# Performance work log

Hardware: AMD Instinct MI355X
Metric: run time of the kernel (lower is better)

Reference implementation:

```python
import jax, jax.numpy as jnp
import numpy as np

EPS = 1e-5
NEG_SLOPE = 0.2


def knn(x, k):
    # x: (B, C, N). pairwise_distance = -||xi - xj||^2, topk -> nearest neighbors.
    xt = jnp.swapaxes(x, 1, 2)                       # (B, N, C)
    inner = -2.0 * jnp.matmul(xt, x)                 # (B, N, N)
    xx = jnp.sum(x * x, axis=1, keepdims=True)       # (B, 1, N)
    pd = -xx - inner - jnp.swapaxes(xx, 1, 2)        # (B, N, N)
    return jax.lax.top_k(pd, k)[1]                   # (B, N, k) int32


def get_graph_feature(x, k):
    # x: (B, C, N) -> (B, N, k, 2C) edge features [neighbor - center, center]
    idx = knn(x, k)
    xt = jnp.swapaxes(x, 1, 2)                       # (B, N, C)
    nb = jax.vmap(lambda f, i: f[i])(xt, idx)        # (B, N, k, C) gather
    center = xt[:, :, None, :]                       # (B, N, 1, C)
    return jnp.concatenate(
        [nb - center, jnp.broadcast_to(center, nb.shape)], axis=-1)


def edge_conv(x, w, k):
    # conv_2d with kernel 1: 1x1 conv (no bias) + InstanceNorm2d + LeakyReLU, then max over k
    feat = get_graph_feature(x, k)                   # (B, N, k, 2C)
    y = jnp.einsum('bnkc,oc->bonk', feat, w)         # (B, O, N, k)
    mean = jnp.mean(y, axis=(2, 3), keepdims=True)
    var = jnp.var(y, axis=(2, 3), keepdims=True)
    y = (y - mean) * jax.lax.rsqrt(var + EPS)        # InstanceNorm2d (no affine)
    y = jnp.where(y >= 0, y, NEG_SLOPE * y)
    return jnp.max(y, axis=-1)                       # (B, O, N)


def setup_inputs() -> dict:
    key = jax.random.key(0)
    ks = jax.random.split(key, 8)
    B, N = 16, 2048
    s = 0.05
    return {
        'x': jax.random.normal(ks[0], (B, 3, N), dtype=jnp.float32),
        'w1': jax.random.normal(ks[1], (64, 6), dtype=jnp.float32) * s,
        'w2': jax.random.normal(ks[2], (64, 128), dtype=jnp.float32) * s,
        'w3': jax.random.normal(ks[3], (128, 128), dtype=jnp.float32) * s,
        'w4': jax.random.normal(ks[4], (256, 256), dtype=jnp.float32) * s,
        'w5': jax.random.normal(ks[5], (512, 512), dtype=jnp.float32) * s,
        'bn5_gamma': jnp.ones((512,), dtype=jnp.float32),
        'bn5_beta': jnp.zeros((512,), dtype=jnp.float32),
    }


def reference(x, w1, w2, w3, w4, w5, bn5_gamma, bn5_beta):
    k = 20
    x1 = edge_conv(x, w1, k)                         # (B, 64, N)
    x2 = edge_conv(x1, w2, k)                        # (B, 64, N)
    x3 = edge_conv(x2, w3, k)                        # (B, 128, N)
    x4 = edge_conv(x3, w4, k)                        # (B, 256, N)
    x_cat = jnp.concatenate([x1, x2, x3, x4], axis=1)  # (B, 512, N)
    y = jnp.einsum('bcn,oc->bon', x_cat, w5)         # conv5, (B, 512, N)
    # BatchNorm1d (training-mode batch stats) over (B, N)
    mean = jnp.mean(y, axis=(0, 2), keepdims=True)
    var = jnp.var(y, axis=(0, 2), keepdims=True)
    y = (y - mean) * jax.lax.rsqrt(var + EPS)
    y = y * bn5_gamma[None, :, None] + bn5_beta[None, :, None]
    y = jnp.where(y >= 0, y, NEG_SLOPE * y)
    feat = jnp.concatenate([jnp.max(y, axis=2), jnp.mean(y, axis=2)], axis=1)  # (B, 1024)
    return feat
```

## Files before the change

kernel.cpp:

```cpp
#include <hip/hip_runtime.h>

#define NN 2048
#define NB 16
#define KK 20
#define EPSF 1e-5f

typedef unsigned long long ull;
typedef _Float16 v8h __attribute__((ext_vector_type(8)));
typedef float v4f __attribute__((ext_vector_type(4)));

__device__ __forceinline__ float shflx_f(float v, int m) { return __shfl_xor(v, m, 64); }
__device__ __forceinline__ ull shflx_u64(ull v, int m) {
  int lo = __shfl_xor((int)(unsigned)v, m, 64);
  int hi = __shfl_xor((int)(unsigned)(v >> 32), m, 64);
  return (((ull)(unsigned)hi) << 32) | (unsigned)lo;
}
__device__ __forceinline__ ull packkey(float s, int n) {
  unsigned u = __float_as_uint(s);
  u = (u & 0x80000000u) ? ~u : (u | 0x80000000u);
  return (((ull)u) << 32) | (unsigned)(2047 - n);
}

__global__ __launch_bounds__(256) void prep_kernel(const float* __restrict__ x,
    _Float16* __restrict__ xh, _Float16* __restrict__ xl, float* __restrict__ xx,
    int C, int KB, long bstride)
{
  const int b = blockIdx.y;
  const int n = blockIdx.x * 256 + threadIdx.x;
  const float* xb = x + (size_t)b * bstride;
  const int Cp = KB * 32;
  _Float16* ph = xh + ((size_t)b * NN + n) * Cp;
  _Float16* pl = xl + ((size_t)b * NN + n) * Cp;
  float s = 0.f;
  for (int kb = 0; kb < KB; kb++) {
    for (int g = 0; g < 4; g++) {
      v8h hv, lv;
#pragma unroll
      for (int j = 0; j < 8; j++) {
        int c = kb * 32 + g * 8 + j;
        float v = (c < C) ? xb[(size_t)c * NN + n] : 0.f;
        _Float16 h = (_Float16)v;
        hv[j] = h;
        lv[j] = (_Float16)(v - (float)h);
        s = fmaf(v, v, s);
      }
      *(v8h*)(ph + kb * 32 + g * 8) = hv;
      *(v8h*)(pl + kb * 32 + g * 8) = lv;
    }
  }
  xx[b * NN + n] = s;
}

template<int KB>
__device__ __forceinline__ void tile_scores(const v8h (&Bh)[KB], const v8h (&Bl)[KB],
    const v8h (&Ah)[4][KB], const v8h (&Al)[4][KB], float xv, v4f (&out)[4])
{
#pragma unroll
  for (int a = 0; a < 4; a++) {
    v4f a0 = {0.f, 0.f, 0.f, 0.f};
    v4f a1 = {0.f, 0.f, 0.f, 0.f};
#pragma unroll
    for (int kb = 0; kb < KB; kb++) {
      v4f& acc = (kb & 1) ? a1 : a0;
      acc = __builtin_amdgcn_mfma_f32_16x16x32_f16(Ah[a][kb], Bh[kb], acc, 0, 0, 0);
      acc = __builtin_amdgcn_mfma_f32_16x16x32_f16(Ah[a][kb], Bl[kb], acc, 0, 0, 0);
      acc = __builtin_amdgcn_mfma_f32_16x16x32_f16(Al[a][kb], Bh[kb], acc, 0, 0, 0);
    }
    v4f s = a0 + a1;
#pragma unroll
    for (int j = 0; j < 4; j++) out[a][j] = s[j] - 0.5f * xv;
  }
}

template<int KB>
__global__ __launch_bounds__(256, 1) void knn2(
    const _Float16* __restrict__ xh, const _Float16* __restrict__ xl,
    const float* __restrict__ xxg, ull* __restrict__ slistG, int* __restrict__ cntG)
{
  __shared__ float gmL[256][33];
  __shared__ float tauL[256];
  __shared__ int scnt[256];

  const int t = threadIdx.x;
  const int lane = t & 63;
  const int wave = t >> 6;
  const int col = lane & 15;
  const int quad = lane >> 4;
  const int quad8 = quad * 8;
  const int b = blockIdx.x >> 1;
  const int chunk = blockIdx.x & 1;
  const int qg = blockIdx.y;
  const int Cp = KB * 32;
  const int cb = chunk * 1024;
  const _Float16* xhb = xh + (size_t)b * NN * Cp;
  const _Float16* xlb = xl + (size_t)b * NN * Cp;
  const float* xxb = xxg + b * NN;

  v8h Ah[4][KB], Al[4][KB];
  const int qw = qg * 256 + wave * 64;
#pragma unroll
  for (int a = 0; a < 4; a++) {
    const _Float16* pa = xhb + (size_t)(qw + a * 16 + col) * Cp + quad8;
    const _Float16* pb = xlb + (size_t)(qw + a * 16 + col) * Cp + quad8;
#pragma unroll
    for (int kb = 0; kb < KB; kb++) {
      Ah[a][kb] = *(const v8h*)(pa + kb * 32);
      Al[a][kb] = *(const v8h*)(pb + kb * 32);
    }
  }

  v8h Bh[2][KB], Bl[2][KB];
  float xvb[2];
  auto loadB = [&](int slot, int tt) {
    int t2 = tt < 63 ? tt : 63;
    int n = cb + t2 * 16 + col;
    const _Float16* pb = xhb + (size_t)n * Cp + quad8;
    const _Float16* pl = xlb + (size_t)n * Cp + quad8;
#pragma unroll
    for (int kb = 0; kb < KB; kb++) {
      Bh[slot][kb] = *(const v8h*)(pb + kb * 32);
      Bl[slot][kb] = *(const v8h*)(pl + kb * 32);
    }
    xvb[slot] = xxb[n];
  };

  float gm[4][8];
#pragma unroll
  for (int a = 0; a < 4; a++)
#pragma unroll
    for (int j = 0; j < 8; j++) gm[a][j] = -3.4e38f;

  loadB(0, 0);
  for (int tt = 0; tt < 64; tt += 2) {
    loadB(1, tt + 1);
    {
      v4f out[4];
      tile_scores<KB>(Bh[0], Bl[0], Ah, Al, xvb[0], out);
#pragma unroll
      for (int a = 0; a < 4; a++)
#pragma unroll
        for (int j = 0; j < 4; j++) gm[a][j * 2] = fmaxf(gm[a][j * 2], out[a][j]);
    }
    loadB(0, tt + 2);
    {
      v4f out[4];
      tile_scores<KB>(Bh[1], Bl[1], Ah, Al, xvb[1], out);
#pragma unroll
      for (int a = 0; a < 4; a++)
#pragma unroll
        for (int j = 0; j < 4; j++) gm[a][j * 2 + 1] = fmaxf(gm[a][j * 2 + 1], out[a][j]);
    }
  }

#pragma unroll
  for (int a = 0; a < 4; a++)
#pragma unroll
    for (int j = 0; j < 4; j++) {
      int qi = wave * 64 + a * 16 + quad * 4 + j;
      gmL[qi][col * 2 + 0] = gm[a][j * 2 + 0];
      gmL[qi][col * 2 + 1] = gm[a][j * 2 + 1];
    }
  scnt[t] = 0;
  asm volatile("s_waitcnt lgkmcnt(0)" ::: "memory");

  for (int r = 0; r < 32; r++) {
    const int q = wave * 64 + r * 2 + (lane >> 5);
    const int idx = lane & 31;
    float v = gmL[q][idx];
#pragma unroll
    for (int kk = 2; kk <= 32; kk <<= 1) {
#pragma unroll
      for (int m = kk >> 1; m >= 1; m >>= 1) {
        float o = shflx_f(v, m);
        bool keepmax = ((idx & kk) == 0) == ((idx & m) == 0);
        v = keepmax ? fmaxf(v, o) : fminf(v, o);
      }
    }
    if (idx == 19) tauL[q] = v;
  }
  asm volatile("s_waitcnt lgkmcnt(0)" ::: "memory");

  float tq[4][4];
#pragma unroll
  for (int a = 0; a < 4; a++)
#pragma unroll
    for (int j = 0; j < 4; j++) tq[a][j] = tauL[wave * 64 + a * 16 + quad * 4 + j];

  ull* slB = slistG + (((size_t)b * NN + qg * 256) * 2 + chunk) * 64;
  loadB(0, 0);
  for (int tt = 0; tt < 64; tt += 2) {
    loadB(1, tt + 1);
    for (int s = 0; s < 2; s++) {
      v4f out[4];
      tile_scores<KB>(s ? Bh[1] : Bh[0], s ? Bl[1] : Bl[0], Ah, Al, xvb[s], out);
      int n = cb + (tt + s) * 16 + col;
#pragma unroll
      for (int a = 0; a < 4; a++)
#pragma unroll
        for (int j = 0; j < 4; j++) {
          float sc = out[a][j];
          if (sc >= tq[a][j]) {
            int qi = wave * 64 + a * 16 + quad * 4 + j;
            int pos = atomicAdd(&scnt[qi], 1);
            if (pos < 64) slB[(size_t)qi * 128 + pos] = packkey(sc, n);
          }
        }
      if (s == 0) loadB(0, tt + 2);
    }
  }
  asm volatile("s_waitcnt lgkmcnt(0)" ::: "memory");
  cntG[((size_t)b * NN + qg * 256 + t) * 2 + chunk] = scnt[t];
}

__global__ __launch_bounds__(256) void knn_merge(const ull* __restrict__ slistG,
    const int* __restrict__ cntG, const _Float16* __restrict__ xh,
    const _Float16* __restrict__ xl, const float* __restrict__ xxg,
    int* __restrict__ idxout, int Cp, int C)
{
  const int lane = threadIdx.x & 63, wave = threadIdx.x >> 6;
  const int b = blockIdx.y;
  const int q = blockIdx.x * 4 + wave;
  const int c0 = cntG[((size_t)b * NN + q) * 2 + 0];
  const int c1 = cntG[((size_t)b * NN + q) * 2 + 1];
  int* op = idxout + ((size_t)b * NN + q) * KK;

  if (c0 <= 64 && c1 <= 64) {
    const ull* s0 = slistG + ((size_t)b * NN + q) * 128;
    const int total = c0 + c1;
    ull e0 = 0, e1 = 0;
    int p0 = lane, p1 = lane + 64;
    if (p0 < total) e0 = (p0 < c0) ? s0[p0] : s0[64 + p0 - c0];
    if (p1 < total) e1 = (p1 < c0) ? s0[p1] : s0[64 + p1 - c0];
    for (int s = 0; s < KK; s++) {
      ull m = e0 > e1 ? e0 : e1;
      ull g = m;
#pragma unroll
      for (int d = 1; d < 64; d <<= 1) { ull o = shflx_u64(g, d); g = o > g ? o : g; }
      if (lane == 0) op[s] = 2047 - (int)(g & 0xFFFFFFFFu);
      if (e0 == g) e0 = 0; else if (e1 == g) e1 = 0;
    }
  } else {
    const _Float16* qh = xh + ((size_t)b * NN + q) * Cp;
    const _Float16* ql = xl + ((size_t)b * NN + q) * Cp;
    const float* xxb = xxg + b * NN;
    float sc[32];
#pragma unroll
    for (int i = 0; i < 32; i++) sc[i] = -0.5f * xxb[lane + 64 * i];
    for (int c = 0; c < C; c++) {
      float qv = (float)qh[c] + (float)ql[c];
      for (int i = 0; i < 32; i++) {
        int n = lane + 64 * i;
        float bv = (float)xh[((size_t)b * NN + n) * Cp + c] + (float)xl[((size_t)b * NN + n) * Cp + c];
        sc[i] = fmaf(qv, bv, sc[i]);
      }
    }
    for (int s = 0; s < KK; s++) {
      ull m = 0; int mi = -1;
      for (int i = 0; i < 32; i++) {
        ull k = packkey(sc[i], lane + 64 * i);
        if (k > m) { m = k; mi = i; }
      }
      ull g = m;
#pragma unroll
      for (int d = 1; d < 64; d <<= 1) { ull o = shflx_u64(g, d); g = o > g ? o : g; }
      if (lane == 0) op[s] = 2047 - (int)(g & 0xFFFFFFFFu);
      if (m == g && mi >= 0) sc[mi] = -3.4e38f;
    }
  }
}

__global__ __launch_bounds__(256) void wcvt_uv(const float* __restrict__ w,
    _Float16* __restrict__ wuh, _Float16* __restrict__ wul,
    _Float16* __restrict__ wvh, _Float16* __restrict__ wvl, int C, int Cp, int O)
{
  int idx = blockIdx.x * 256 + threadIdx.x;
  if (idx >= O * Cp) return;
  int o = idx / Cp, c = idx - o * Cp;
  float a = 0.f, bv = 0.f;
  if (c < C) { a = w[o * 2 * C + c]; bv = w[o * 2 * C + C + c]; }
  float v = bv - a;
  _Float16 ah = (_Float16)a; wuh[idx] = ah; wul[idx] = (_Float16)(a - (float)ah);
  _Float16 vh = (_Float16)v; wvh[idx] = vh; wvl[idx] = (_Float16)(v - (float)vh);
}

__global__ __launch_bounds__(256) void w5cvt(const float* __restrict__ w5,
    _Float16* __restrict__ w5h, _Float16* __restrict__ w5l)
{
  int idx = blockIdx.x * 256 + threadIdx.x;
  float v = w5[idx];
  _Float16 h = (_Float16)v;
  w5h[idx] = h;
  w5l[idx] = (_Float16)(v - (float)h);
}

__global__ __launch_bounds__(256) void y5cvt_kernel(const float* __restrict__ xcat,
    _Float16* __restrict__ xh, _Float16* __restrict__ xl)
{
  const int b = blockIdx.y;
  const int n = blockIdx.x * 256 + threadIdx.x;
  for (int kc = blockIdx.z * 4; kc < blockIdx.z * 4 + 4; kc++) {
    v8h h[4], l[4];
#pragma unroll
    for (int g = 0; g < 4; g++)
#pragma unroll
      for (int j = 0; j < 8; j++) {
        float v = xcat[((size_t)b * 512 + kc * 32 + g * 8 + j) * NN + n];
        _Float16 hh = (_Float16)v;
        h[g][j] = hh;
        l[g][j] = (_Float16)(v - (float)hh);
      }
    size_t base = (((size_t)b * 16 + kc) * NN + n) * 32;
#pragma unroll
    for (int g = 0; g < 4; g++) {
      *(v8h*)(xh + base + g * 8) = h[g];
      *(v8h*)(xl + base + g * 8) = l[g];
    }
  }
}

__global__ __launch_bounds__(256) void y5_mfma(const _Float16* __restrict__ w5h,
    const _Float16* __restrict__ w5l, const _Float16* __restrict__ xh,
    const _Float16* __restrict__ xl, float* __restrict__ y5)
{
  const int lane = threadIdx.x & 63, wave = threadIdx.x >> 6;
  const int col = lane & 15, quad = lane >> 4, quad8 = quad * 8;
  const int b = blockIdx.z;
  const int o0 = blockIdx.x * 256 + wave * 64;
  const int nb0 = blockIdx.y * 128;
  v4f acc[4][8];
#pragma unroll
  for (int a = 0; a < 4; a++)
#pragma unroll
    for (int t = 0; t < 8; t++) acc[a][t] = {0.f, 0.f, 0.f, 0.f};

  for (int kc = 0; kc < 16; kc++) {
    v8h Ah[4], Al[4];
#pragma unroll
    for (int a = 0; a < 4; a++) {
      size_t off = (size_t)(o0 + a * 16 + col) * 512 + kc * 32 + quad8;
      Ah[a] = *(const v8h*)(w5h + off);
      Al[a] = *(const v8h*)(w5l + off);
    }
#pragma unroll
    for (int t = 0; t < 8; t++) {
      int n = nb0 + t * 16 + col;
      size_t boff = (((size_t)b * 16 + kc) * NN + n) * 32 + quad8;
      v8h Bh = *(const v8h*)(xh + boff);
      v8h Bl = *(const v8h*)(xl + boff);
#pragma unroll
      for (int a = 0; a < 4; a++) {
        acc[a][t] = __builtin_amdgcn_mfma_f32_16x16x32_f16(Ah[a], Bh, acc[a][t], 0, 0, 0);
        acc[a][t] = __builtin_amdgcn_mfma_f32_16x16x32_f16(Ah[a], Bl, acc[a][t], 0, 0, 0);
        acc[a][t] = __builtin_amdgcn_mfma_f32_16x16x32_f16(Al[a], Bh, acc[a][t], 0, 0, 0);
      }
    }
  }
#pragma unroll
  for (int a = 0; a < 4; a++)
#pragma unroll
    for (int t = 0; t < 8; t++)
#pragma unroll
      for (int j = 0; j < 4; j++)
        y5[((size_t)b * 512 + o0 + a * 16 + quad * 4 + j) * NN + nb0 + t * 16 + col] = acc[a][t][j];
}

__global__ __launch_bounds__(256) void uv_mfma(const _Float16* __restrict__ wuh,
    const _Float16* __restrict__ wul, const _Float16* __restrict__ wvh,
    const _Float16* __restrict__ wvl, const _Float16* __restrict__ xh,
    const _Float16* __restrict__ xl, float* __restrict__ Uc, float* __restrict__ Vc,
    int Cp)
{
  const int lane = threadIdx.x & 63, wave = threadIdx.x >> 6;
  const int col = lane & 15, quad = lane >> 4, quad8 = quad * 8;
  const int b = blockIdx.z;
  const int o0 = blockIdx.x * 32;
  const int nb0 = blockIdx.y * 512 + wave * 128;
  v4f aU[2][8], aV[2][8];
#pragma unroll
  for (int a = 0; a < 2; a++)
#pragma unroll
    for (int t = 0; t < 8; t++) { aU[a][t] = {0.f,0.f,0.f,0.f}; aV[a][t] = {0.f,0.f,0.f,0.f}; }

  const int KBr = Cp >> 5;
  for (int kb = 0; kb < KBr; kb++) {
    v8h Uh[2], Ul[2], Vh[2], Vl[2];
#pragma unroll
    for (int a = 0; a < 2; a++) {
      size_t off = (size_t)(o0 + a * 16 + col) * Cp + kb * 32 + quad8;
      Uh[a] = *(const v8h*)(wuh + off);
      Ul[a] = *(const v8h*)(wul + off);
      Vh[a] = *(const v8h*)(wvh + off);
      Vl[a] = *(const v8h*)(wvl + off);
    }
#pragma unroll
    for (int t = 0; t < 8; t++) {
      int n = nb0 + t * 16 + col;
      size_t boff = ((size_t)b * NN + n) * Cp + kb * 32 + quad8;
      v8h Bh = *(const v8h*)(xh + boff);
      v8h Bl = *(const v8h*)(xl + boff);
#pragma unroll
      for (int a = 0; a < 2; a++) {
        aU[a][t] = __builtin_amdgcn_mfma_f32_16x16x32_f16(Uh[a], Bh, aU[a][t], 0, 0, 0);
        aU[a][t] = __builtin_amdgcn_mfma_f32_16x16x32_f16(Uh[a], Bl, aU[a][t], 0, 0, 0);
        aU[a][t] = __builtin_amdgcn_mfma_f32_16x16x32_f16(Ul[a], Bh, aU[a][t], 0, 0, 0);
        aV[a][t] = __builtin_amdgcn_mfma_f32_16x16x32_f16(Vh[a], Bh, aV[a][t], 0, 0, 0);
        aV[a][t] = __builtin_amdgcn_mfma_f32_16x16x32_f16(Vh[a], Bl, aV[a][t], 0, 0, 0);
        aV[a][t] = __builtin_amdgcn_mfma_f32_16x16x32_f16(Vl[a], Bh, aV[a][t], 0, 0, 0);
      }
    }
  }
#pragma unroll
  for (int a = 0; a < 2; a++)
#pragma unroll
    for (int t = 0; t < 8; t++)
#pragma unroll
      for (int j = 0; j < 4; j++) {
        size_t base = ((size_t)b * 64 + o0 + a * 16 + quad * 4 + j) * NN + nb0 + t * 16 + col;
        Uc[base] = aU[a][t][j];
        Vc[base] = aV[a][t][j];
      }
}

__global__ __launch_bounds__(256) void edge_kernel(const float* __restrict__ Uc,
    const float* __restrict__ Vc, const int* __restrict__ idx,
    float* __restrict__ xo)
{
  __shared__ float Ur[4 * 2052];
  __shared__ float red[8][4];
  __shared__ float smv[8];
  const int b = blockIdx.y, o0 = blockIdx.x * 4;
  const int t = threadIdx.x, lane = t & 63, wave = t >> 6;
  for (int r = 0; r < 4; r++)
    for (int i = t; i < NN; i += 256)
      Ur[r * 2052 + i] = Uc[((size_t)b * 64 + o0 + r) * NN + i];
  __syncthreads();
  const float* Vb = Vc + ((size_t)b * 64 + o0) * NN;
  const int* ib = idx + (size_t)b * NN * KK;
  float s0 = 0, s1 = 0, s2 = 0, s3 = 0, c0 = 0, c1 = 0, c2 = 0, c3 = 0;
  for (int n = t; n < NN; n += 256) {
    float v0 = Vb[n], v1 = Vb[NN + n], v2 = Vb[2 * NN + n], v3 = Vb[3 * NN + n];
    const int* ip = ib + (size_t)n * KK;
#pragma unroll
    for (int j = 0; j < KK; j++) {
      int m = ip[j];
      float y0 = Ur[m] + v0, y1 = Ur[2052 + m] + v1;
      float y2 = Ur[4104 + m] + v2, y3 = Ur[6156 + m] + v3;
      s0 += y0; c0 = fmaf(y0, y0, c0);
      s1 += y1; c1 = fmaf(y1, y1, c1);
      s2 += y2; c2 = fmaf(y2, y2, c2);
      s3 += y3; c3 = fmaf(y3, y3, c3);
    }
  }
  float sa[4] = { s0, s1, s2, s3 }, ca[4] = { c0, c1, c2, c3 };
#pragma unroll
  for (int r = 0; r < 4; r++) {
    float a = sa[r], c = ca[r];
#pragma unroll
    for (int d = 1; d < 64; d <<= 1) { a += shflx_f(a, d); c += shflx_f(c, d); }
    if (lane == 0) { red[r][wave] = a; red[4 + r][wave] = c; }
  }
  __syncthreads();
  if (t < 4) {
    float a = red[t][0] + red[t][1] + red[t][2] + red[t][3];
    float c = red[4 + t][0] + red[4 + t][1] + red[4 + t][2] + red[4 + t][3];
    const float inv = 1.f / (float)(NN * KK);
    float mu = a * inv;
    float var = fmaxf(c * inv - mu * mu, 0.f);
    smv[t] = mu;
    smv[4 + t] = rsqrtf(var + EPSF);
  }
  __syncthreads();
  const float mu0 = smv[0], mu1 = smv[1], mu2 = smv[2], mu3 = smv[3];
  const float i0 = smv[4], i1 = smv[5], i2 = smv[6], i3 = smv[7];
  for (int n = t; n < NN; n += 256) {
    float v0 = Vb[n], v1 = Vb[NN + n], v2 = Vb[2 * NN + n], v3 = Vb[3 * NN + n];
    const int* ip = ib + (size_t)n * KK;
    float m0 = -3.4e38f, m1 = m0, m2 = m0, m3 = m0;
#pragma unroll
    for (int j = 0; j < KK; j++) {
      int m = ip[j];
      m0 = fmaxf(m0, Ur[m] + v0);
      m1 = fmaxf(m1, Ur[2052 + m] + v1);
      m2 = fmaxf(m2, Ur[4104 + m] + v2);
      m3 = fmaxf(m3, Ur[6156 + m] + v3);
    }
    float z;
    z = (m0 - mu0) * i0; xo[((size_t)b * 512 + o0 + 0) * NN + n] = z >= 0.f ? z : 0.2f * z;
    z = (m1 - mu1) * i1; xo[((size_t)b * 512 + o0 + 1) * NN + n] = z >= 0.f ? z : 0.2f * z;
    z = (m2 - mu2) * i2; xo[((size_t)b * 512 + o0 + 2) * NN + n] = z >= 0.f ? z : 0.2f * z;
    z = (m3 - mu3) * i3; xo[((size_t)b * 512 + o0 + 3) * NN + n] = z >= 0.f ? z : 0.2f * z;
  }
}

__global__ __launch_bounds__(256) void bn5stat_kernel(const float* __restrict__ y5,
    float* __restrict__ bn5) {
  __shared__ float rs[4], rq[4];
  const int o = blockIdx.x, t = threadIdx.x, lane = t & 63, wave = t >> 6;
  float s = 0.f, q = 0.f;
  for (int b = 0; b < NB; b++) {
    const float* p = y5 + ((size_t)b * 512 + o) * NN;
    for (int n = t; n < NN; n += 256) { float v = p[n]; s += v; q = fmaf(v, v, q); }
  }
#pragma unroll
  for (int d = 1; d < 64; d <<= 1) { s += shflx_f(s, d); q += shflx_f(q, d); }
  if (lane == 0) { rs[wave] = s; rq[wave] = q; }
  __syncthreads();
  if (t == 0) {
    float S = rs[0] + rs[1] + rs[2] + rs[3];
    float Q = rq[0] + rq[1] + rq[2] + rq[3];
    const float inv = 1.f / (float)(NB * NN);
    float mu = S * inv;
    float var = fmaxf(Q * inv - mu * mu, 0.f);
    bn5[o] = mu;
    bn5[512 + o] = rsqrtf(var + EPSF);
  }
}

__global__ __launch_bounds__(256) void final_kernel(const float* __restrict__ y5,
    const float* __restrict__ bn5, const float* __restrict__ gamma,
    const float* __restrict__ beta, float* __restrict__ out)
{
  __shared__ float rm[4], rs[4];
  const int o = blockIdx.x, b = blockIdx.y, t = threadIdx.x, lane = t & 63, wave = t >> 6;
  const float mu = bn5[o], iv = bn5[512 + o], g = gamma[o], be = beta[o];
  const float* p = y5 + ((size_t)b * 512 + o) * NN;
  float mx = -3.4e38f, sm = 0.f;
  for (int n = t; n < NN; n += 256) {
    float z = (p[n] - mu) * iv;
    z = z * g + be;
    z = (z >= 0.f) ? z : 0.2f * z;
    mx = fmaxf(mx, z);
    sm += z;
  }
#pragma unroll
  for (int d = 1; d < 64; d <<= 1) { mx = fmaxf(mx, shflx_f(mx, d)); sm += shflx_f(sm, d); }
  if (lane == 0) { rm[wave] = mx; rs[wave] = sm; }
  __syncthreads();
  if (t == 0) {
    float M = fmaxf(fmaxf(rm[0], rm[1]), fmaxf(rm[2], rm[3]));
    float S = rs[0] + rs[1] + rs[2] + rs[3];
    out[(size_t)b * 1024 + o] = M;
    out[(size_t)b * 1024 + 512 + o] = S * (1.f / NN);
  }
}

extern "C" void kernel_launch(void* const* d_in, const int* in_sizes, int n_in,
                              void* d_out, int out_size, void* d_ws, size_t ws_size,
                              hipStream_t stream)
{
  (void)in_sizes; (void)n_in; (void)out_size; (void)ws_size;
  const float* x  = (const float*)d_in[0];
  const float* w1 = (const float*)d_in[1];
  const float* w2 = (const float*)d_in[2];
  const float* w3 = (const float*)d_in[3];
  const float* w4 = (const float*)d_in[4];
  const float* w5 = (const float*)d_in[5];
  const float* g5 = (const float*)d_in[6];
  const float* b5 = (const float*)d_in[7];
  float* out = (float*)d_out;

  float* ws   = (float*)d_ws;
  float* xcat = ws;
  float* Ub   = xcat + 16777216;
  float* Vb   = Ub + 8388608;
  int*   idxb = (int*)(Vb + 8388608);
  float* xxb  = (float*)(idxb + 655360);
  float* bn5  = xxb + 32768;

  _Float16* xth = (_Float16*)Vb;
  _Float16* xtl = xth + (size_t)NB * NN * 128;
  int* cntb = (int*)(Vb + 4194304);
  float* Vc = Vb + 4259840;
  _Float16* wuh = (_Float16*)(Vb + 6356992);
  _Float16* wul = wuh + 32768;
  _Float16* wvh = wul + 32768;
  _Float16* wvl = wvh + 32768;

  ull* slist = (ull*)Ub;
  float* Uc = Ub;

  _Float16* w5h = (_Float16*)idxb;
  _Float16* w5l = w5h + 262144;
  _Float16* xcfh = (_Float16*)Ub;
  _Float16* xcfl = (_Float16*)Vb;
  float* y5 = xcat;

  struct Lyr { const float* xin; long bstride; int C, KB, O, coff; const float* w; };
  const Lyr L[4] = {
    { x,              3L * NN,   3,   1, 64,  0,   w1 },
    { xcat,           512L * NN, 64,  2, 64,  64,  w2 },
    { xcat + 64 * NN, 512L * NN, 64,  2, 128, 128, w3 },
    { xcat + 128 * NN,512L * NN, 128, 4, 256, 256, w4 },
  };

  for (int l = 0; l < 4; l++) {
    const int Cp = L[l].KB * 32, O = L[l].O;
    prep_kernel<<<dim3(NN / 256, NB), 256, 0, stream>>>(L[l].xin, xth, xtl, xxb,
                                                        L[l].C, L[l].KB, L[l].bstride);
    switch (L[l].KB) {
      case 1: knn2<1><<<dim3(NB * 2, NN / 256), 256, 0, stream>>>(xth, xtl, xxb, slist, cntb); break;
      case 2: knn2<2><<<dim3(NB * 2, NN / 256), 256, 0, stream>>>(xth, xtl, xxb, slist, cntb); break;
      default: knn2<4><<<dim3(NB * 2, NN / 256), 256, 0, stream>>>(xth, xtl, xxb, slist, cntb); break;
    }
    knn_merge<<<dim3(NN / 4, NB), 256, 0, stream>>>(slist, cntb, xth, xtl, xxb, idxb,
                                                    Cp, L[l].C);
    wcvt_uv<<<(O * Cp + 255) / 256, 256, 0, stream>>>(L[l].w, wuh, wul, wvh, wvl,
                                                      L[l].C, Cp, O);
    for (int c0 = 0; c0 < O; c0 += 64) {
      uv_mfma<<<dim3(2, NN / 512, NB), 256, 0, stream>>>(
          wuh + (size_t)c0 * Cp, wul + (size_t)c0 * Cp,
          wvh + (size_t)c0 * Cp, wvl + (size_t)c0 * Cp,
          xth, xtl, Uc, Vc, Cp);
      edge_kernel<<<dim3(16, NB), 256, 0, stream>>>(Uc, Vc, idxb,
          xcat + (size_t)(L[l].coff + c0) * NN);
    }
  }
  w5cvt<<<1024, 256, 0, stream>>>(w5, w5h, w5l);
  y5cvt_kernel<<<dim3(NN / 256, NB, 4), 256, 0, stream>>>(xcat, xcfh, xcfl);
  y5_mfma<<<dim3(2, NN / 128, NB), 256, 0, stream>>>(w5h, w5l, xcfh, xcfl, y5);
  bn5stat_kernel<<<512, 256, 0, stream>>>(y5, bn5);
  final_kernel<<<dim3(512, NB), 256, 0, stream>>>(y5, bn5, g5, b5, out);
}
```

Measured before the change: 1.743 ms.

## Widen edge-conv channel chunks and shrink per-block work for more parallelism

```diff
diff --git a/kernel.cpp b/kernel.cpp
--- a/kernel.cpp
+++ b/kernel.cpp
@@ -368,18 +368,18 @@
     const _Float16* __restrict__ wul, const _Float16* __restrict__ wvh,
     const _Float16* __restrict__ wvl, const _Float16* __restrict__ xh,
     const _Float16* __restrict__ xl, float* __restrict__ Uc, float* __restrict__ Vc,
-    int Cp)
+    int Cp, int Och)
 {
   const int lane = threadIdx.x & 63, wave = threadIdx.x >> 6;
   const int col = lane & 15, quad = lane >> 4, quad8 = quad * 8;
   const int b = blockIdx.z;
   const int o0 = blockIdx.x * 32;
-  const int nb0 = blockIdx.y * 512 + wave * 128;
-  v4f aU[2][8], aV[2][8];
+  const int nb0 = blockIdx.y * 256 + wave * 64;
+  v4f aU[2][4], aV[2][4];
 #pragma unroll
   for (int a = 0; a < 2; a++)
 #pragma unroll
-    for (int t = 0; t < 8; t++) { aU[a][t] = {0.f,0.f,0.f,0.f}; aV[a][t] = {0.f,0.f,0.f,0.f}; }
+    for (int t = 0; t < 4; t++) { aU[a][t] = {0.f,0.f,0.f,0.f}; aV[a][t] = {0.f,0.f,0.f,0.f}; }
 
   const int KBr = Cp >> 5;
   for (int kb = 0; kb < KBr; kb++) {
@@ -393,7 +393,7 @@
       Vl[a] = *(const v8h*)(wvl + off);
     }
 #pragma unroll
-    for (int t = 0; t < 8; t++) {
+    for (int t = 0; t < 4; t++) {
       int n = nb0 + t * 16 + col;
       size_t boff = ((size_t)b * NN + n) * Cp + kb * 32 + quad8;
       v8h Bh = *(const v8h*)(xh + boff);
@@ -412,83 +412,75 @@
 #pragma unroll
   for (int a = 0; a < 2; a++)
 #pragma unroll
-    for (int t = 0; t < 8; t++)
+    for (int t = 0; t < 4; t++)
 #pragma unroll
       for (int j = 0; j < 4; j++) {
-        size_t base = ((size_t)b * 64 + o0 + a * 16 + quad * 4 + j) * NN + nb0 + t * 16 + col;
+        size_t base = ((size_t)b * Och + o0 + a * 16 + quad * 4 + j) * NN + nb0 + t * 16 + col;
         Uc[base] = aU[a][t][j];
         Vc[base] = aV[a][t][j];
       }
 }
 
-__global__ __launch_bounds__(256) void edge_kernel(const float* __restrict__ Uc,
+__global__ __launch_bounds__(256) void edge5(const float* __restrict__ Uc,
     const float* __restrict__ Vc, const int* __restrict__ idx,
-    float* __restrict__ xo)
-{
-  __shared__ float Ur[4 * 2052];
-  __shared__ float red[8][4];
-  __shared__ float smv[8];
-  const int b = blockIdx.y, o0 = blockIdx.x * 4;
+    float* __restrict__ xo, int Och)
+{
+  __shared__ float Ur[2 * 2052];
+  __shared__ float red[4][4];
+  __shared__ float smv[4];
+  const int b = blockIdx.y, o0 = blockIdx.x * 2;
   const int t = threadIdx.x, lane = t & 63, wave = t >> 6;
-  for (int r = 0; r < 4; r++)
+  for (int r = 0; r < 2; r++)
     for (int i = t; i < NN; i += 256)
-      Ur[r * 2052 + i] = Uc[((size_t)b * 64 + o0 + r) * NN + i];
+      Ur[r * 2052 + i] = Uc[((size_t)b * Och + o0 + r) * NN + i];
   __syncthreads();
-  const float* Vb = Vc + ((size_t)b * 64 + o0) * NN;
+  const float* Vp = Vc + ((size_t)b * Och + o0) * NN;
   const int* ib = idx + (size_t)b * NN * KK;
-  float s0 = 0, s1 = 0, s2 = 0, s3 = 0, c0 = 0, c1 = 0, c2 = 0, c3 = 0;
+  float s0 = 0, s1 = 0, c0 = 0, c1 = 0;
   for (int n = t; n < NN; n += 256) {
-    float v0 = Vb[n], v1 = Vb[NN + n], v2 = Vb[2 * NN + n], v3 = Vb[3 * NN + n];
+    float v0 = Vp[n], v1 = Vp[NN + n];
     const int* ip = ib + (size_t)n * KK;
 #pragma unroll
     for (int j = 0; j < KK; j++) {
       int m = ip[j];
       float y0 = Ur[m] + v0, y1 = Ur[2052 + m] + v1;
-      float y2 = Ur[4104 + m] + v2, y3 = Ur[6156 + m] + v3;
       s0 += y0; c0 = fmaf(y0, y0, c0);
       s1 += y1; c1 = fmaf(y1, y1, c1);
-      s2 += y2; c2 = fmaf(y2, y2, c2);
-      s3 += y3; c3 = fmaf(y3, y3, c3);
-    }
-  }
-  float sa[4] = { s0, s1, s2, s3 }, ca[4] = { c0, c1, c2, c3 };
-#pragma unroll
-  for (int r = 0; r < 4; r++) {
-    float a = sa[r], c = ca[r];
-#pragma unroll
-    for (int d = 1; d < 64; d <<= 1) { a += shflx_f(a, d); c += shflx_f(c, d); }
-    if (lane == 0) { red[r][wave] = a; red[4 + r][wave] = c; }
+    }
+  }
+  float st[4] = { s0, s1, c0, c1 };
+#pragma unroll
+  for (int k = 0; k < 4; k++) {
+    float a = st[k];
+#pragma unroll
+    for (int d = 1; d < 64; d <<= 1) a += shflx_f(a, d);
+    if (lane == 0) red[k][wave] = a;
   }
   __syncthreads();
-  if (t < 4) {
+  if (t < 2) {
     float a = red[t][0] + red[t][1] + red[t][2] + red[t][3];
-    float c = red[4 + t][0] + red[4 + t][1] + red[4 + t][2] + red[4 + t][3];
+    float c = red[2 + t][0] + red[2 + t][1] + red[2 + t][2] + red[2 + t][3];
     const float inv = 1.f / (float)(NN * KK);
     float mu = a * inv;
     float var = fmaxf(c * inv - mu * mu, 0.f);
     smv[t] = mu;
-    smv[4 + t] = rsqrtf(var + EPSF);
+    smv[2 + t] = rsqrtf(var + EPSF);
   }
   __syncthreads();
-  const float mu0 = smv[0], mu1 = smv[1], mu2 = smv[2], mu3 = smv[3];
-  const float i0 = smv[4], i1 = smv[5], i2 = smv[6], i3 = smv[7];
+  const float mu0 = smv[0], mu1 = smv[1], i0 = smv[2], i1 = smv[3];
   for (int n = t; n < NN; n += 256) {
-    float v0 = Vb[n], v1 = Vb[NN + n], v2 = Vb[2 * NN + n], v3 = Vb[3 * NN + n];
+    float v0 = Vp[n], v1 = Vp[NN + n];
     const int* ip = ib + (size_t)n * KK;
-    float m0 = -3.4e38f, m1 = m0, m2 = m0, m3 = m0;
+    float m0 = -3.4e38f, m1 = m0;
 #pragma unroll
     for (int j = 0; j < KK; j++) {
       int m = ip[j];
       m0 = fmaxf(m0, Ur[m] + v0);
       m1 = fmaxf(m1, Ur[2052 + m] + v1);
-      m2 = fmaxf(m2, Ur[4104 + m] + v2);
-      m3 = fmaxf(m3, Ur[6156 + m] + v3);
     }
     float z;
     z = (m0 - mu0) * i0; xo[((size_t)b * 512 + o0 + 0) * NN + n] = z >= 0.f ? z : 0.2f * z;
     z = (m1 - mu1) * i1; xo[((size_t)b * 512 + o0 + 1) * NN + n] = z >= 0.f ? z : 0.2f * z;
-    z = (m2 - mu2) * i2; xo[((size_t)b * 512 + o0 + 2) * NN + n] = z >= 0.f ? z : 0.2f * z;
-    z = (m3 - mu3) * i3; xo[((size_t)b * 512 + o0 + 3) * NN + n] = z >= 0.f ? z : 0.2f * z;
   }
 }
 
@@ -568,16 +560,16 @@
   float* bn5  = xxb + 32768;
 
   _Float16* xth = (_Float16*)Vb;
-  _Float16* xtl = xth + (size_t)NB * NN * 128;
+  _Float16* xtl = xth + 4194304;
   int* cntb = (int*)(Vb + 4194304);
-  float* Vc = Vb + 4259840;
-  _Float16* wuh = (_Float16*)(Vb + 6356992);
+  _Float16* wuh = (_Float16*)(Vb + 4259840);
   _Float16* wul = wuh + 32768;
   _Float16* wvh = wul + 32768;
   _Float16* wvl = wvh + 32768;
 
   ull* slist = (ull*)Ub;
   float* Uc = Ub;
+  float* Vc = Ub + 4194304;
 
   _Float16* w5h = (_Float16*)idxb;
   _Float16* w5l = w5h + 262144;
@@ -594,25 +586,26 @@
   };
 
   for (int l = 0; l < 4; l++) {
-    const int Cp = L[l].KB * 32, O = L[l].O;
+    const int Cp = L[l].KB * 32, O = L[l].O, C = L[l].C;
     prep_kernel<<<dim3(NN / 256, NB), 256, 0, stream>>>(L[l].xin, xth, xtl, xxb,
-                                                        L[l].C, L[l].KB, L[l].bstride);
+                                                        C, L[l].KB, L[l].bstride);
     switch (L[l].KB) {
       case 1: knn2<1><<<dim3(NB * 2, NN / 256), 256, 0, stream>>>(xth, xtl, xxb, slist, cntb); break;
       case 2: knn2<2><<<dim3(NB * 2, NN / 256), 256, 0, stream>>>(xth, xtl, xxb, slist, cntb); break;
       default: knn2<4><<<dim3(NB * 2, NN / 256), 256, 0, stream>>>(xth, xtl, xxb, slist, cntb); break;
     }
     knn_merge<<<dim3(NN / 4, NB), 256, 0, stream>>>(slist, cntb, xth, xtl, xxb, idxb,
-                                                    Cp, L[l].C);
+                                                    Cp, C);
     wcvt_uv<<<(O * Cp + 255) / 256, 256, 0, stream>>>(L[l].w, wuh, wul, wvh, wvl,
-                                                      L[l].C, Cp, O);
-    for (int c0 = 0; c0 < O; c0 += 64) {
-      uv_mfma<<<dim3(2, NN / 512, NB), 256, 0, stream>>>(
+                                                      C, Cp, O);
+    for (int c0 = 0; c0 < O; c0 += 128) {
+      const int Och = (O - c0) < 128 ? (O - c0) : 128;
+      uv_mfma<<<dim3(Och / 32, NN / 256, NB), 256, 0, stream>>>(
           wuh + (size_t)c0 * Cp, wul + (size_t)c0 * Cp,
           wvh + (size_t)c0 * Cp, wvl + (size_t)c0 * Cp,
-          xth, xtl, Uc, Vc, Cp);
-      edge_kernel<<<dim3(16, NB), 256, 0, stream>>>(Uc, Vc, idxb,
-          xcat + (size_t)(L[l].coff + c0) * NN);
+          xth, xtl, Uc, Vc, Cp, Och);
+      edge5<<<dim3(Och / 2, NB), 256, 0, stream>>>(Uc, Vc, idxb,
+          xcat + (size_t)(L[l].coff + c0) * NN, Och);
     }
   }
   w5cvt<<<1024, 256, 0, stream>>>(w5, w5h, w5l);
```

Result: faster. 1.636 ms (-6.1%).
